# Optimization experiments

Hardware: AMD Instinct MI355X
Metric: run time of the kernel (lower is better)

Reference implementation:

```python
import jax, jax.numpy as jnp
import numpy as np

B, L, D = 2, 4096, 2048
H, K = 32, 16              # num_heads, mini_batch_size
HD = D // H                # head_dim = 64
NMB = L // K               # 256 mini-batches
TTT_BASE_LR = 1.0
LN_EPS = 1e-6


def setup_inputs() -> dict:
    key = jax.random.key(0)
    ks = jax.random.split(key, 16)
    r = lambda k, s: 0.02 * jax.random.normal(k, s, dtype=jnp.float32)
    return {
        "hidden_states": jax.random.normal(ks[0], (B, L, D), dtype=jnp.float32),
        "wq_w": r(ks[1], (D, D)), "wq_b": r(ks[2], (D,)),
        "wk_w": r(ks[3], (D, D)), "wk_b": r(ks[4], (D,)),
        "wv_w": r(ks[5], (D, D)), "wv_b": r(ks[6], (D,)),
        "wo_w": r(ks[7], (D, D)), "wo_b": r(ks[8], (D,)),
        "ttt_norm_weight": 1.0 + r(ks[9], (H, HD)),
        "ttt_norm_bias": r(ks[10], (H, HD)),
        "lr_w": r(ks[11], (H, 1, D)),       # learnable_ttt_lr_weight
        "lr_b": r(ks[12], (H, 1)),          # learnable_ttt_lr_bias
        "W1": r(ks[13], (H, HD, HD)),
        "b1": r(ks[14], (H, 1, HD)),
        "post_norm_w": jnp.ones((D,), jnp.float32),
        "post_norm_b": jnp.zeros((D,), jnp.float32),
    }


def ln_fwd(x, gamma, beta, eps=LN_EPS):
    mu = x.mean(-1, keepdims=True)
    var = ((x - mu) ** 2).mean(-1, keepdims=True)
    return gamma * ((x - mu) / jnp.sqrt(var + eps)) + beta


def ln_fused_l2_bwd(x, l2_target, gamma, beta, eps=LN_EPS):
    # grad of 0.5*||LN(x)*gamma+beta - target||^2 w.r.t. x (standard TTT helper)
    Dd = x.shape[-1]
    mu = x.mean(-1, keepdims=True)
    var = ((x - mu) ** 2).mean(-1, keepdims=True)
    std = jnp.sqrt(var + eps)
    x_hat = (x - mu) / std
    grad_x_hat = (gamma * x_hat + beta - l2_target) * gamma
    return (Dd * grad_x_hat
            - grad_x_hat.sum(-1, keepdims=True)
            - x_hat * (x_hat * grad_x_hat).sum(-1, keepdims=True)) / (Dd * std)


def reference(hidden_states, wq_w, wq_b, wk_w, wk_b, wv_w, wv_b, wo_w, wo_b,
              ttt_norm_weight, ttt_norm_bias, lr_w, lr_b, W1, b1,
              post_norm_w, post_norm_b):
    # QKV projections
    XQ = (hidden_states @ wq_w + wq_b).reshape(B, L, H, HD)
    XK = (hidden_states @ wk_w + wk_b).reshape(B, L, H, HD)
    XV = (hidden_states @ wv_w + wv_b).reshape(B, L, H, HD)
    # L2 normalize q/k per head (F.normalize, eps=1e-12)
    XQ = XQ / jnp.maximum(jnp.linalg.norm(XQ, axis=-1, keepdims=True), 1e-12)
    XK = XK / jnp.maximum(jnp.linalg.norm(XK, axis=-1, keepdims=True), 1e-12)
    # ln_reconstruction_target: torch.std is unbiased (ddof=1), eps added to std
    diff = XV - XK
    mu = diff.mean(-1, keepdims=True)
    std = jnp.std(diff, axis=-1, ddof=1, keepdims=True)
    XV = (ttt_norm_weight[None, None] * ((diff - mu) / (std + 1e-8))
          + ttt_norm_bias[None, None]) + XK
    # reshape to mini-batches: [B,H,NMB,K,HD]
    Xmb = hidden_states.reshape(B, NMB, K, D)
    tohd = lambda t: t.transpose(0, 2, 1, 3).reshape(B, H, NMB, K, HD)
    XQ, XK, XV = tohd(XQ), tohd(XK), tohd(XV)
    # eta gate: einsum('bnkc,hdc->bhnkd') with d==1, sigmoid, scale
    ttt_lr = jnp.einsum('bnkc,hdc->bhnkd', Xmb, lr_w) + lr_b.reshape(1, H, 1, 1, 1)
    ttt_lr = jax.nn.sigmoid(ttt_lr).transpose(0, 1, 2, 4, 3) * (TTT_BASE_LR / HD)  # [B,H,NMB,1,K]
    eta = jnp.broadcast_to(ttt_lr / K, (B, H, NMB, K, K))
    ln_w = ttt_norm_weight[:, None, :]  # [H,1,HD]
    ln_b = ttt_norm_bias[:, None, :]
    tril = jnp.tril(jnp.ones((K, K), jnp.float32))
    W1s = jnp.broadcast_to(W1[None], (B, H, HD, HD))
    b1s = jnp.broadcast_to(b1[None], (B, H, 1, HD))

    def step(carry, xs):
        W1c, b1c = carry
        xq, xk, xv, eta_mb = xs  # [B,H,K,HD], eta [B,H,K,K]
        Z1 = xk @ W1c + b1c
        grad = ln_fused_l2_bwd(Z1, xv - xk, ln_w, ln_b)        # [B,H,K,HD]
        Attn1 = tril * (xq @ xk.transpose(0, 1, 3, 2))         # causal within mini-batch
        b1_bar = b1c - (tril * eta_mb) @ grad
        Z1_bar = xq @ W1c - (eta_mb * Attn1) @ grad + b1_bar
        last_eta = eta_mb[:, :, -1, :, None]                   # [B,H,K,1]
        W1n = W1c - (last_eta * xk).transpose(0, 1, 3, 2) @ grad
        b1n = b1c - jnp.sum(last_eta * grad, axis=-2, keepdims=True)
        out = xq + ln_fwd(Z1_bar, ln_w, ln_b)
        return (W1n, b1n), out

    xs = tuple(t.transpose(2, 0, 1, 3, 4) for t in (XQ, XK, XV, eta))
    _, outs = jax.lax.scan(step, (W1s, b1s), xs)               # [NMB,B,H,K,HD]
    y = outs.transpose(1, 0, 3, 2, 4).reshape(B, L, D)
    # post_norm LayerNorm(eps=1e-6) then output projection
    mu = y.mean(-1, keepdims=True)
    var = ((y - mu) ** 2).mean(-1, keepdims=True)
    y = (y - mu) / jnp.sqrt(var + 1e-6) * post_norm_w + post_norm_b
    return y @ wo_w + wo_b
```

## Files before the change

### kernel.cpp

```cpp
#include <hip/hip_runtime.h>
#include <hip/hip_bf16.h>
#include <cstdint>
#include <cstddef>

#define DEV __device__ __forceinline__

constexpr int Bb = 2, Ls = 4096, Dd = 2048, Hh = 32, HD = 64, MBK = 16, NMBc = 256;
constexpr int MTOK = Bb * Ls;

typedef __bf16 bf16x8 __attribute__((ext_vector_type(8)));
typedef float  f32x4  __attribute__((ext_vector_type(4)));

DEV unsigned short f2bf(float f) {
    union { __bf16 h; unsigned short u; } x;
    x.h = (__bf16)f;
    return x.u;
}
DEV float b2f(unsigned short u) {
    union { unsigned int i; float f; } x; x.i = ((unsigned int)u) << 16;
    return x.f;
}

DEV float wsum64(float v) {
    int t;
    t = __builtin_amdgcn_update_dpp(0, __float_as_int(v), 0x111, 0xf, 0xf, true); v += __int_as_float(t);
    t = __builtin_amdgcn_update_dpp(0, __float_as_int(v), 0x112, 0xf, 0xf, true); v += __int_as_float(t);
    t = __builtin_amdgcn_update_dpp(0, __float_as_int(v), 0x114, 0xf, 0xf, true); v += __int_as_float(t);
    t = __builtin_amdgcn_update_dpp(0, __float_as_int(v), 0x118, 0xf, 0xf, true); v += __int_as_float(t);
    t = __builtin_amdgcn_update_dpp(0, __float_as_int(v), 0x142, 0xa, 0xf, true); v += __int_as_float(t);
    t = __builtin_amdgcn_update_dpp(0, __float_as_int(v), 0x143, 0xc, 0xf, true); v += __int_as_float(t);
    return __int_as_float(__builtin_amdgcn_readlane(__float_as_int(v), 63));
}

DEV float rsum16(float v) {
    int t;
    t = __builtin_amdgcn_update_dpp(0, __float_as_int(v), 0x121, 0xf, 0xf, true); v += __int_as_float(t);
    t = __builtin_amdgcn_update_dpp(0, __float_as_int(v), 0x122, 0xf, 0xf, true); v += __int_as_float(t);
    t = __builtin_amdgcn_update_dpp(0, __float_as_int(v), 0x124, 0xf, 0xf, true); v += __int_as_float(t);
    t = __builtin_amdgcn_update_dpp(0, __float_as_int(v), 0x128, 0xf, 0xf, true); v += __int_as_float(t);
    return v;
}

DEV float qsum4(float v) {
    int t;
    t = __builtin_amdgcn_update_dpp(0, __float_as_int(v), 0xB1, 0xf, 0xf, true); v += __int_as_float(t);
    t = __builtin_amdgcn_update_dpp(0, __float_as_int(v), 0x4E, 0xf, 0xf, true); v += __int_as_float(t);
    return v;
}

DEV float sel4(int n, float a, float b, float c, float d) {
    float v = (n == 1) ? b : a;
    v = (n == 2) ? c : v;
    v = (n == 3) ? d : v;
    return v;
}

DEV void g2l16(const void* g, void* l) {
    __builtin_amdgcn_global_load_lds(
        (__attribute__((address_space(1))) void*)(g),
        (__attribute__((address_space(3))) void*)(l), 16, 0, 0);
}

__global__ __launch_bounds__(256) void cast_hs_kernel(const float* __restrict__ src,
                                                      unsigned short* __restrict__ dst) {
    int i = (blockIdx.x * 256 + threadIdx.x) * 4;
    float4 v = *(const float4*)(src + i);
    ushort4 o; o.x = f2bf(v.x); o.y = f2bf(v.y); o.z = f2bf(v.z); o.w = f2bf(v.w);
    *(ushort4*)(dst + i) = o;
}

__global__ __launch_bounds__(256) void transpose_cast_kernel(const float* __restrict__ W,
                                                             unsigned short* __restrict__ Wt) {
    __shared__ float tile[64][65];
    int bx = blockIdx.x & 31;
    int by = blockIdx.x >> 5;
    int t = threadIdx.x;
    int r = t >> 4, c4 = (t & 15) * 4;
    #pragma unroll
    for (int i = 0; i < 4; ++i) {
        int row = r + i * 16;
        float4 v = *(const float4*)(W + (size_t)(bx * 64 + row) * Dd + by * 64 + c4);
        tile[row][c4 + 0] = v.x; tile[row][c4 + 1] = v.y;
        tile[row][c4 + 2] = v.z; tile[row][c4 + 3] = v.w;
    }
    __syncthreads();
    #pragma unroll
    for (int i = 0; i < 4; ++i) {
        int row = r + i * 16;
        ushort4 o;
        o.x = f2bf(tile[c4 + 0][row]); o.y = f2bf(tile[c4 + 1][row]);
        o.z = f2bf(tile[c4 + 2][row]); o.w = f2bf(tile[c4 + 3][row]);
        *(ushort4*)(Wt + (size_t)(by * 64 + row) * Dd + bx * 64 + c4) = o;
    }
}

__global__ __launch_bounds__(256) void gemm_bt_kernel(const unsigned short* __restrict__ A,
                                                      const unsigned short* __restrict__ Bt,
                                                      const float* __restrict__ bias,
                                                      float* __restrict__ C,
                                                      int M, int N, int Kd) {
    __shared__ unsigned short sA[128 * 64];
    __shared__ unsigned short sB[128 * 64];
    int t = threadIdx.x;
    int lane = t & 63;
    int wid = t >> 6, wm = wid >> 1, wn = wid & 1;
    int quad = lane >> 4, c = lane & 15;
    int bm = blockIdx.x, bn = blockIdx.y;

    const unsigned short* pa[4]; const unsigned short* pb[4];
    unsigned short* la[4]; unsigned short* lb[4];
    #pragma unroll
    for (int i = 0; i < 4; ++i) {
        int lin = i * 256 + t;
        int row = lin >> 3, blk = lin & 7;
        int oct = blk ^ (row & 7);
        pa[i] = A  + (size_t)(bm * 128 + row) * Kd + oct * 8;
        pb[i] = Bt + (size_t)(bn * 128 + row) * Kd + oct * 8;
        la[i] = sA + lin * 8;
        lb[i] = sB + lin * 8;
    }

    f32x4 acc[4][4];
    #pragma unroll
    for (int i = 0; i < 4; ++i)
        #pragma unroll
        for (int j = 0; j < 4; ++j)
            #pragma unroll
            for (int r = 0; r < 4; ++r) acc[i][j][r] = 0.f;

    const char* sAc = (const char*)sA;
    const char* sBc = (const char*)sB;
    int rowA0 = wm * 64 + c, rowB0 = wn * 64 + c;
    int sw = (c & 7);

    int nkt = Kd >> 6;
    for (int kt = 0; kt < nkt; ++kt) {
        #pragma unroll
        for (int i = 0; i < 4; ++i) {
            g2l16(pa[i], la[i]);
            g2l16(pb[i], lb[i]);
            pa[i] += 64; pb[i] += 64;
        }
        __syncthreads();
        #pragma unroll
        for (int s = 0; s < 2; ++s) {
            bf16x8 af[4], bfv[4];
            int so = (s << 2) | quad;
            #pragma unroll
            for (int mt = 0; mt < 4; ++mt)
                af[mt] = *(const bf16x8*)(sAc + (rowA0 + mt * 16) * 128 + ((so ^ sw) * 16));
            #pragma unroll
            for (int nt = 0; nt < 4; ++nt)
                bfv[nt] = *(const bf16x8*)(sBc + (rowB0 + nt * 16) * 128 + ((so ^ sw) * 16));
            #pragma unroll
            for (int mt = 0; mt < 4; ++mt)
                #pragma unroll
                for (int nt = 0; nt < 4; ++nt)
                    acc[mt][nt] = __builtin_amdgcn_mfma_f32_16x16x32_bf16(af[mt], bfv[nt], acc[mt][nt], 0, 0, 0);
        }
        __syncthreads();
    }

    float bv[4];
    #pragma unroll
    for (int nt = 0; nt < 4; ++nt) bv[nt] = bias[bn * 128 + wn * 64 + nt * 16 + c];
    #pragma unroll
    for (int mt = 0; mt < 4; ++mt)
        #pragma unroll
        for (int r = 0; r < 4; ++r) {
            int row = bm * 128 + wm * 64 + mt * 16 + quad * 4 + r;
            float* cp = C + (size_t)row * N + bn * 128 + wn * 64 + c;
            #pragma unroll
            for (int nt = 0; nt < 4; ++nt) cp[nt * 16] = acc[mt][nt][r] + bv[nt];
        }
}

__global__ __launch_bounds__(256) void lr_kernel(const float* __restrict__ hs,
                                                 const float* __restrict__ lrw,
                                                 const float* __restrict__ lrb,
                                                 float* __restrict__ lr_out) {
    int tok = blockIdx.x;
    int t = threadIdx.x;
    int h = t >> 3, j0 = t & 7;
    const float* row = hs + (size_t)tok * Dd;
    const float* wr = lrw + (size_t)h * Dd;
    float p = 0.f;
    for (int j = j0 * 4; j < Dd; j += 32) {
        float4 a = *(const float4*)(row + j);
        float4 w = *(const float4*)(wr + j);
        p += a.x * w.x + a.y * w.y + a.z * w.z + a.w * w.w;
    }
    __shared__ float red[32][8];
    red[h][j0] = p;
    __syncthreads();
    if (t < 32) {
        float s = 0.f;
        #pragma unroll
        for (int i = 0; i < 8; ++i) s += red[t][i];
        s += lrb[t];
        s = 1.f / (1.f + expf(-s));
        s *= 1.0f / (HD * MBK);
        int b = tok >> 12, l = tok & (Ls - 1);
        lr_out[(size_t)(b * Hh + t) * Ls + l] = s;
    }
}

__global__ __launch_bounds__(256) void attn_kernel(const float* __restrict__ XQ,
                                                   const float* __restrict__ XK,
                                                   const float* __restrict__ lrbuf,
                                                   unsigned short* __restrict__ attG) {
    __shared__ unsigned short qb[4][16 * 72];
    __shared__ unsigned short kb[4][16 * 72];
    int t = threadIdx.x, w = t >> 6, lane = t & 63;
    int gid = blockIdx.x * 4 + w;
    int bh = gid >> 8, nmb = gid & 255;
    int b = bh >> 5, h = bh & 31;
    int l0 = nmb * 16;
    int tok = lane >> 2, fq = lane & 3;
    size_t base = ((size_t)(b * Ls) + l0 + tok) * Dd + h * 64 + fq * 16;
    float4 qv[4], kv[4];
    #pragma unroll
    for (int i = 0; i < 4; ++i) {
        qv[i] = *(const float4*)(XQ + base + 4 * i);
        kv[i] = *(const float4*)(XK + base + 4 * i);
    }
    float sq = 0.f, sk = 0.f;
    #pragma unroll
    for (int i = 0; i < 4; ++i) {
        sq += qv[i].x * qv[i].x + qv[i].y * qv[i].y + qv[i].z * qv[i].z + qv[i].w * qv[i].w;
        sk += kv[i].x * kv[i].x + kv[i].y * kv[i].y + kv[i].z * kv[i].z + kv[i].w * kv[i].w;
    }
    float rq = 1.f / fmaxf(sqrtf(qsum4(sq)), 1e-12f);
    float rk = 1.f / fmaxf(sqrtf(qsum4(sk)), 1e-12f);
    #pragma unroll
    for (int i = 0; i < 4; ++i) {
        ushort4 oq, ok;
        oq.x = f2bf(qv[i].x * rq); oq.y = f2bf(qv[i].y * rq);
        oq.z = f2bf(qv[i].z * rq); oq.w = f2bf(qv[i].w * rq);
        ok.x = f2bf(kv[i].x * rk); ok.y = f2bf(kv[i].y * rk);
        ok.z = f2bf(kv[i].z * rk); ok.w = f2bf(kv[i].w * rk);
        *(ushort4*)&qb[w][tok * 72 + fq * 16 + 4 * i] = oq;
        *(ushort4*)&kb[w][tok * 72 + fq * 16 + 4 * i] = ok;
    }
    __syncthreads();
    int q2 = lane >> 4, n = lane & 15;
    bf16x8 qf0 = *(const bf16x8*)&qb[w][n * 72 + 8 * q2];
    bf16x8 qf1 = *(const bf16x8*)&qb[w][n * 72 + 32 + 8 * q2];
    bf16x8 kf0 = *(const bf16x8*)&kb[w][n * 72 + 8 * q2];
    bf16x8 kf1 = *(const bf16x8*)&kb[w][n * 72 + 32 + 8 * q2];
    const f32x4 zero4 = {0.f, 0.f, 0.f, 0.f};
    f32x4 a = __builtin_amdgcn_mfma_f32_16x16x32_bf16(qf1, kf1, zero4, 0, 0, 0);
    a = __builtin_amdgcn_mfma_f32_16x16x32_bf16(qf0, kf0, a, 0, 0, 0);
    float svn = lrbuf[(size_t)bh * Ls + l0 + n];
    unsigned short* op = attG + ((size_t)bh * NMBc + nmb) * 256;
    #pragma unroll
    for (int r = 0; r < 4; ++r) {
        int i = 4 * q2 + r;
        float v = (i >= n) ? (-svn * (a[r] + 1.f)) : 0.f;
        op[i * 16 + n] = f2bf(v);
    }
}

DEV void stage_qkv(float4 q, float4 k, float4 v,
                   float* tq, float* tk, float* tv,
                   unsigned short* bq, unsigned short* bk,
                   int rowp, int c4p, float4 lnw4, float4 lnb4) {
    float rq = 1.f / fmaxf(sqrtf(rsum16(q.x*q.x + q.y*q.y + q.z*q.z + q.w*q.w)), 1e-12f);
    q.x *= rq; q.y *= rq; q.z *= rq; q.w *= rq;
    float rk = 1.f / fmaxf(sqrtf(rsum16(k.x*k.x + k.y*k.y + k.z*k.z + k.w*k.w)), 1e-12f);
    k.x *= rk; k.y *= rk; k.z *= rk; k.w *= rk;
    float4 df; df.x = v.x - k.x; df.y = v.y - k.y; df.z = v.z - k.z; df.w = v.w - k.w;
    float mu = rsum16(df.x + df.y + df.z + df.w) * (1.f / 64.f);
    float4 cc; cc.x = df.x - mu; cc.y = df.y - mu; cc.z = df.z - mu; cc.w = df.w - mu;
    float var = rsum16(cc.x*cc.x + cc.y*cc.y + cc.z*cc.z + cc.w*cc.w) * (1.f / 63.f);
    float rs = 1.f / (sqrtf(var) + 1e-8f);
    float4 vn;
    vn.x = lnw4.x * cc.x * rs + lnb4.x + k.x;
    vn.y = lnw4.y * cc.y * rs + lnb4.y + k.y;
    vn.z = lnw4.z * cc.z * rs + lnb4.z + k.z;
    vn.w = lnw4.w * cc.w * rs + lnb4.w + k.w;
    *(float4*)&tq[rowp * 68 + c4p] = q;
    *(float4*)&tk[rowp * 68 + c4p] = k;
    *(float4*)&tv[rowp * 68 + c4p] = vn;
    ushort4 qb, kb;
    qb.x = f2bf(q.x); qb.y = f2bf(q.y); qb.z = f2bf(q.z); qb.w = f2bf(q.w);
    kb.x = f2bf(k.x); kb.y = f2bf(k.y); kb.z = f2bf(k.z); kb.w = f2bf(k.w);
    *(ushort4*)&bq[rowp * 72 + c4p] = qb;
    *(ushort4*)&bk[rowp * 72 + c4p] = kb;
}

__global__ __launch_bounds__(256, 1) void scan_kernel(const float* __restrict__ XQ,
                                                      const float* __restrict__ XK,
                                                      const float* __restrict__ XV,
                                                      const float* __restrict__ lrbuf,
                                                      const unsigned short* __restrict__ attG,
                                                      const float* __restrict__ W1in,
                                                      const float* __restrict__ b1in,
                                                      const float* __restrict__ lnw_g,
                                                      const float* __restrict__ lnb_g,
                                                      float* __restrict__ Y) {
    int bh = blockIdx.x;
    int b = bh >> 5, h = bh & 31;
    int t = threadIdx.x;
    int w = t >> 6;
    int lane = t & 63;
    int q = lane >> 4, n = lane & 15;
    int gc = 16 * w + n;

    __shared__ float tiles[2][3][16 * 68];
    __shared__ unsigned short tbq[2][16 * 72];
    __shared__ unsigned short tbk[2][16 * 72];
    __shared__ float svb[2][16];
    __shared__ unsigned short wt_hi[64 * 72];
    __shared__ unsigned short wt_lo[64 * 72];
    __shared__ float zTr[16 * 68];
    __shared__ unsigned short gbufT[64 * 32];
    __shared__ unsigned short sxkT[64 * 32];
    __shared__ unsigned short attb[16 * 32];
    __shared__ float pb[4 * 64];
    __shared__ float s1p[16 * 4], s2p[16 * 4];
    __shared__ float s1z[16 * 4], s2z[16 * 4];

    #pragma unroll
    for (int i = 0; i < 16; ++i) {
        int k = i * 4 + w;
        float val = W1in[(size_t)h * 4096 + (size_t)k * 64 + lane];
        unsigned short hi = f2bf(val);
        unsigned short lo = f2bf(val - b2f(hi));
        wt_hi[lane * 72 + k] = hi;
        wt_lo[lane * 72 + k] = lo;
    }
    #pragma unroll
    for (int i = 0; i < 8; ++i) { gbufT[i * 256 + t] = 0; sxkT[i * 256 + t] = 0; }
    #pragma unroll
    for (int i = 0; i < 2; ++i) attb[i * 256 + t] = 0;

    float b1r = b1in[h * 64 + lane];
    float b1c = b1in[h * 64 + gc];
    float lnwr = lnw_g[h * 64 + lane];
    float lnbr = lnb_g[h * 64 + lane];
    float lnwc = lnw_g[h * 64 + gc];
    float lnbc = lnb_g[h * 64 + gc];

    const size_t gbase = ((size_t)b * Ls) * Dd + h * 64;
    const float* lrp = lrbuf + (size_t)bh * Ls;
    const unsigned short* attp_base = attG + (size_t)bh * NMBc * 256;
    int arow = 4 * w + (lane >> 2), ac4 = (lane & 3) * 4;

    int rowp = t >> 4, c4p = (t & 15) * 4;
    float4 lnw4 = *(const float4*)(lnw_g + h * 64 + c4p);
    float4 lnb4 = *(const float4*)(lnb_g + h * 64 + c4p);

    {
        float4 q0 = *(const float4*)(XQ + gbase + (size_t)rowp * Dd + c4p);
        float4 k0 = *(const float4*)(XK + gbase + (size_t)rowp * Dd + c4p);
        float4 v0 = *(const float4*)(XV + gbase + (size_t)rowp * Dd + c4p);
        stage_qkv(q0, k0, v0, &tiles[0][0][0], &tiles[0][1][0], &tiles[0][2][0],
                  tbq[0], tbk[0], rowp, c4p, lnw4, lnb4);
    }
    if (t < 16) svb[0][t] = lrp[t];
    float4 preq = *(const float4*)(XQ + gbase + (size_t)(16 + rowp) * Dd + c4p);
    float4 prek = *(const float4*)(XK + gbase + (size_t)(16 + rowp) * Dd + c4p);
    float4 prev = *(const float4*)(XV + gbase + (size_t)(16 + rowp) * Dd + c4p);
    float presv = (t < 16) ? lrp[16 + t] : 0.f;
    ushort4 attp = {0, 0, 0, 0};
    if (lane < 16) attp = *(const ushort4*)(attp_base + arow * 16 + ac4);
    __syncthreads();

    const f32x4 zero4 = {0.f, 0.f, 0.f, 0.f};

    for (int nmb = 0; nmb < NMBc; ++nmb) {
        int cb = nmb & 1, nb2 = cb ^ 1;
        int l0 = nmb * 16;
        stage_qkv(preq, prek, prev, &tiles[nb2][0][0], &tiles[nb2][1][0], &tiles[nb2][2][0],
                  tbq[nb2], tbk[nb2], rowp, c4p, lnw4, lnb4);
        if (t < 16) svb[nb2][t] = presv;
        if (lane < 16) {
            *(ushort4*)&attb[arow * 32 + ac4] = attp;
            int ap = (nmb + 1 < NMBc) ? (nmb + 1) : (NMBc - 1);
            attp = *(const ushort4*)(attp_base + (size_t)ap * 256 + arow * 16 + ac4);
        }
        int lp = (l0 + 32 <= Ls - 16) ? (l0 + 32) : (Ls - 16);
        preq = *(const float4*)(XQ + gbase + (size_t)(lp + rowp) * Dd + c4p);
        prek = *(const float4*)(XK + gbase + (size_t)(lp + rowp) * Dd + c4p);
        prev = *(const float4*)(XV + gbase + (size_t)(lp + rowp) * Dd + c4p);
        presv = (t < 16) ? lrp[lp + t] : 0.f;

        const float* xqs = &tiles[cb][0][0];
        const float* xks = &tiles[cb][1][0];
        const float* xvs = &tiles[cb][2][0];
        const unsigned short* bqs = tbq[cb];
        const unsigned short* bks = tbk[cb];

        bf16x8 qf0 = *(const bf16x8*)&bqs[n * 72 + 8 * q];
        bf16x8 qf1 = *(const bf16x8*)&bqs[n * 72 + 32 + 8 * q];
        bf16x8 kf0 = *(const bf16x8*)&bks[n * 72 + 8 * q];
        bf16x8 kf1 = *(const bf16x8*)&bks[n * 72 + 32 + 8 * q];

        bf16x8 wh0 = *(const bf16x8*)&wt_hi[gc * 72 + 8 * q];
        bf16x8 wh1 = *(const bf16x8*)&wt_hi[gc * 72 + 32 + 8 * q];
        bf16x8 wl0 = *(const bf16x8*)&wt_lo[gc * 72 + 8 * q];
        bf16x8 wl1 = *(const bf16x8*)&wt_lo[gc * 72 + 32 + 8 * q];

        f32x4 z1 = __builtin_amdgcn_mfma_f32_16x16x32_bf16(kf0, wh0, zero4, 0, 0, 0);
        z1 = __builtin_amdgcn_mfma_f32_16x16x32_bf16(kf1, wh1, z1, 0, 0, 0);
        f32x4 z1l = __builtin_amdgcn_mfma_f32_16x16x32_bf16(kf0, wl0, zero4, 0, 0, 0);
        z1l = __builtin_amdgcn_mfma_f32_16x16x32_bf16(kf1, wl1, z1l, 0, 0, 0);
        z1 = z1 + z1l;
        f32x4 zb = __builtin_amdgcn_mfma_f32_16x16x32_bf16(qf0, wh0, zero4, 0, 0, 0);
        zb = __builtin_amdgcn_mfma_f32_16x16x32_bf16(qf1, wh1, zb, 0, 0, 0);
        f32x4 zbl = __builtin_amdgcn_mfma_f32_16x16x32_bf16(qf0, wl0, zero4, 0, 0, 0);
        zbl = __builtin_amdgcn_mfma_f32_16x16x32_bf16(qf1, wl1, zbl, 0, 0, 0);
        zb = zb + zbl;

        #pragma unroll
        for (int r = 0; r < 4; ++r) zTr[(4 * q + r) * 68 + gc] = z1[r];
        {
            float p1[4], p2[4];
            #pragma unroll
            for (int r = 0; r < 4; ++r) {
                float za = z1[r] + b1c;
                p1[r] = rsum16(za);
                p2[r] = rsum16(za * za);
            }
            if (n < 4) {
                s1p[(4 * q + n) * 4 + w] = sel4(n, p1[0], p1[1], p1[2], p1[3]);
                s2p[(4 * q + n) * 4 + w] = sel4(n, p2[0], p2[1], p2[2], p2[3]);
            }
        }
        __syncthreads();

        float xk_rm[4], xv_rm[4], zar[4];
        #pragma unroll
        for (int r = 0; r < 4; ++r) {
            int rw = 4 * w + r;
            zar[r] = zTr[rw * 68 + lane] + b1r;
            xk_rm[r] = xks[rw * 68 + lane];
            xv_rm[r] = xvs[rw * 68 + lane];
        }
        float4 svr4 = *(const float4*)&svb[cb][4 * w];
        float svr[4] = {svr4.x, svr4.y, svr4.z, svr4.w};
        float gr[4]; float pbv = 0.f;
        #pragma unroll
        for (int r = 0; r < 4; ++r) {
            int rw = 4 * w + r;
            float4 a1 = *(const float4*)&s1p[rw * 4];
            float4 a2 = *(const float4*)&s2p[rw * 4];
            float s1 = a1.x + a1.y + a1.z + a1.w;
            float s2 = a2.x + a2.y + a2.z + a2.w;
            float mu = s1 * (1.f / 64.f);
            float var = s2 * (1.f / 64.f) - mu * mu;
            float rstd = rsqrtf(var + 1e-6f);
            float xh = (zar[r] - mu) * rstd;
            float g = (lnwr * xh + lnbr - (xv_rm[r] - xk_rm[r])) * lnwr;
            float sg = wsum64(g);
            float sxg = wsum64(xh * g);
            gr[r] = (64.f * g - sg - xh * sxg) * rstd * (1.f / 64.f);
            pbv += svr[r] * gr[r];
        }
        {
            ushort4 gp, sp;
            gp.x = f2bf(gr[0]); gp.y = f2bf(gr[1]); gp.z = f2bf(gr[2]); gp.w = f2bf(gr[3]);
            sp.x = f2bf(svr[0] * xk_rm[0]); sp.y = f2bf(svr[1] * xk_rm[1]);
            sp.z = f2bf(svr[2] * xk_rm[2]); sp.w = f2bf(svr[3] * xk_rm[3]);
            *(ushort4*)&gbufT[lane * 32 + 4 * w] = gp;
            *(ushort4*)&sxkT[lane * 32 + 4 * w] = sp;
            pb[w * 64 + lane] = pbv;
        }
        __syncthreads();

        bf16x8 gF = *(const bf16x8*)&gbufT[gc * 32 + 8 * q];
        bf16x8 amF = *(const bf16x8*)&attb[n * 32 + 8 * q];
        zb = __builtin_amdgcn_mfma_f32_16x16x32_bf16(amF, gF, zb, 0, 0, 0);
        float zbar[4], xqc[4];
        {
            float pz1[4], pz2[4];
            #pragma unroll
            for (int r = 0; r < 4; ++r) {
                zbar[r] = zb[r] + b1c;
                pz1[r] = rsum16(zbar[r]);
                pz2[r] = rsum16(zbar[r] * zbar[r]);
                xqc[r] = xqs[(4 * q + r) * 68 + gc];
            }
            if (n < 4) {
                s1z[(4 * q + n) * 4 + w] = sel4(n, pz1[0], pz1[1], pz1[2], pz1[3]);
                s2z[(4 * q + n) * 4 + w] = sel4(n, pz2[0], pz2[1], pz2[2], pz2[3]);
            }
        }
        #pragma unroll
        for (int tm = 0; tm < 4; ++tm) {
            bf16x8 ax = *(const bf16x8*)&sxkT[(16 * tm + n) * 32 + 8 * q];
            f32x4 dl = __builtin_amdgcn_mfma_f32_16x16x32_bf16(ax, gF, zero4, 0, 0, 0);
            int ko = 16 * tm + 4 * q;
            ushort4 h4 = *(ushort4*)&wt_hi[gc * 72 + ko];
            ushort4 l4 = *(ushort4*)&wt_lo[gc * 72 + ko];
            float w0 = b2f(h4.x) + b2f(l4.x) - dl[0];
            float w1 = b2f(h4.y) + b2f(l4.y) - dl[1];
            float w2 = b2f(h4.z) + b2f(l4.z) - dl[2];
            float w3 = b2f(h4.w) + b2f(l4.w) - dl[3];
            h4.x = f2bf(w0); l4.x = f2bf(w0 - b2f(h4.x));
            h4.y = f2bf(w1); l4.y = f2bf(w1 - b2f(h4.y));
            h4.z = f2bf(w2); l4.z = f2bf(w2 - b2f(h4.z));
            h4.w = f2bf(w3); l4.w = f2bf(w3 - b2f(h4.w));
            *(ushort4*)&wt_hi[gc * 72 + ko] = h4;
            *(ushort4*)&wt_lo[gc * 72 + ko] = l4;
        }
        float b1r_n = b1r - (pb[0 * 64 + lane] + pb[64 + lane] +
                             pb[128 + lane] + pb[192 + lane]);
        float b1c_n = b1c - (pb[0 * 64 + gc] + pb[64 + gc] +
                             pb[128 + gc] + pb[192 + gc]);
        __syncthreads();

        #pragma unroll
        for (int r = 0; r < 4; ++r) {
            int row = 4 * q + r;
            float4 a1 = *(const float4*)&s1z[row * 4];
            float4 a2 = *(const float4*)&s2z[row * 4];
            float s1 = a1.x + a1.y + a1.z + a1.w;
            float s2 = a2.x + a2.y + a2.z + a2.w;
            float mu = s1 * (1.f / 64.f);
            float var = s2 * (1.f / 64.f) - mu * mu;
            float rstd = rsqrtf(var + 1e-6f);
            float o = lnwc * ((zbar[r] - mu) * rstd) + lnbc + xqc[r];
            Y[gbase + (size_t)(l0 + row) * Dd + gc] = o;
        }
        b1r = b1r_n; b1c = b1c_n;
    }
}

__global__ __launch_bounds__(256) void postnorm_kernel(const float* __restrict__ Y,
                                                       const float* __restrict__ pw,
                                                       const float* __restrict__ pb,
                                                       unsigned short* __restrict__ Yb) {
    int tok = blockIdx.x, t = threadIdx.x;
    const float* row = Y + (size_t)tok * Dd;
    int c0 = t * 4, c1 = 1024 + t * 4;
    float4 v0 = *(const float4*)(row + c0);
    float4 v1 = *(const float4*)(row + c1);
    float s1 = v0.x + v0.y + v0.z + v0.w + v1.x + v1.y + v1.z + v1.w;
    float s2 = v0.x * v0.x + v0.y * v0.y + v0.z * v0.z + v0.w * v0.w +
               v1.x * v1.x + v1.y * v1.y + v1.z * v1.z + v1.w * v1.w;
    s1 = wsum64(s1); s2 = wsum64(s2);
    __shared__ float r1[4], r2[4];
    if ((t & 63) == 0) { r1[t >> 6] = s1; r2[t >> 6] = s2; }
    __syncthreads();
    float S1 = r1[0] + r1[1] + r1[2] + r1[3];
    float S2 = r2[0] + r2[1] + r2[2] + r2[3];
    float mu = S1 * (1.f / 2048.f);
    float var = S2 * (1.f / 2048.f) - mu * mu;
    float rstd = rsqrtf(var + 1e-6f);
    float4 w0 = *(const float4*)(pw + c0), b0 = *(const float4*)(pb + c0);
    float4 w1 = *(const float4*)(pw + c1), b1 = *(const float4*)(pb + c1);
    ushort4 o0, o1;
    o0.x = f2bf((v0.x - mu) * rstd * w0.x + b0.x);
    o0.y = f2bf((v0.y - mu) * rstd * w0.y + b0.y);
    o0.z = f2bf((v0.z - mu) * rstd * w0.z + b0.z);
    o0.w = f2bf((v0.w - mu) * rstd * w0.w + b0.w);
    o1.x = f2bf((v1.x - mu) * rstd * w1.x + b1.x);
    o1.y = f2bf((v1.y - mu) * rstd * w1.y + b1.y);
    o1.z = f2bf((v1.z - mu) * rstd * w1.z + b1.z);
    o1.w = f2bf((v1.w - mu) * rstd * w1.w + b1.w);
    *(ushort4*)(Yb + (size_t)tok * Dd + c0) = o0;
    *(ushort4*)(Yb + (size_t)tok * Dd + c1) = o1;
}

extern "C" void kernel_launch(void* const* d_in, const int* in_sizes, int n_in,
                              void* d_out, int out_size, void* d_ws, size_t ws_size,
                              hipStream_t stream) {
    const float* hs   = (const float*)d_in[0];
    const float* wq_w = (const float*)d_in[1];
    const float* wq_b = (const float*)d_in[2];
    const float* wk_w = (const float*)d_in[3];
    const float* wk_b = (const float*)d_in[4];
    const float* wv_w = (const float*)d_in[5];
    const float* wv_b = (const float*)d_in[6];
    const float* wo_w = (const float*)d_in[7];
    const float* wo_b = (const float*)d_in[8];
    const float* lnw  = (const float*)d_in[9];
    const float* lnb  = (const float*)d_in[10];
    const float* lr_w = (const float*)d_in[11];
    const float* lr_b = (const float*)d_in[12];
    const float* W1   = (const float*)d_in[13];
    const float* b1   = (const float*)d_in[14];
    const float* pnw  = (const float*)d_in[15];
    const float* pnb  = (const float*)d_in[16];
    float* out = (float*)d_out;

    char* ws = (char*)d_ws;
    size_t off = 0;
    auto alloc = [&](size_t bytes) -> void* {
        void* p = ws + off; off += (bytes + 255) & ~(size_t)255; return p;
    };
    unsigned short* hsb = (unsigned short*)alloc((size_t)MTOK * Dd * 2);
    unsigned short* wtb = (unsigned short*)alloc((size_t)Dd * Dd * 2);
    float* XQ = (float*)alloc((size_t)MTOK * Dd * 4);
    float* XK = (float*)alloc((size_t)MTOK * Dd * 4);
    float* XV = (float*)alloc((size_t)MTOK * Dd * 4);
    float* lrbuf = (float*)alloc((size_t)Bb * Hh * Ls * 4);
    float* Y = XQ;
    unsigned short* Yb = hsb;
    unsigned short* attG = hsb;

    dim3 blk(256);
    cast_hs_kernel<<<dim3(MTOK * Dd / 1024), blk, 0, stream>>>(hs, hsb);

    transpose_cast_kernel<<<dim3(1024), blk, 0, stream>>>(wq_w, wtb);
    gemm_bt_kernel<<<dim3(64, 16), blk, 0, stream>>>(hsb, wtb, wq_b, XQ, MTOK, Dd, Dd);
    transpose_cast_kernel<<<dim3(1024), blk, 0, stream>>>(wk_w, wtb);
    gemm_bt_kernel<<<dim3(64, 16), blk, 0, stream>>>(hsb, wtb, wk_b, XK, MTOK, Dd, Dd);
    transpose_cast_kernel<<<dim3(1024), blk, 0, stream>>>(wv_w, wtb);
    gemm_bt_kernel<<<dim3(64, 16), blk, 0, stream>>>(hsb, wtb, wv_b, XV, MTOK, Dd, Dd);

    lr_kernel<<<dim3(MTOK), blk, 0, stream>>>(hs, lr_w, lr_b, lrbuf);
    attn_kernel<<<dim3(Bb * Hh * NMBc / 4), blk, 0, stream>>>(XQ, XK, lrbuf, attG);

    scan_kernel<<<dim3(Bb * Hh), blk, 0, stream>>>(XQ, XK, XV, lrbuf, attG, W1, b1, lnw, lnb, Y);

    postnorm_kernel<<<dim3(MTOK), blk, 0, stream>>>(Y, pnw, pnb, Yb);

    transpose_cast_kernel<<<dim3(1024), blk, 0, stream>>>(wo_w, wtb);
    gemm_bt_kernel<<<dim3(64, 16), blk, 0, stream>>>(Yb, wtb, wo_b, out, MTOK, Dd, Dd);
}
```

Measured before the change: 1.448 ms.

## Fuse attention-matrix computation into scan kernel and defer output LN store

Removes the separate attn_kernel and its global attG buffer; warp 0 of the scan kernel now computes the masked eta-scaled q·k^T tile with MFMA inside each mini-batch step, into double-buffered shared memory. The final LayerNorm and store of each mini-batch's output is deferred to the next iteration so one __syncthreads per step can be dropped. Prefetch loads for the next tiles are moved later in the loop. This removes one launch and a global round trip, but adds serial MFMA work to the latency-bound scan loop, which runs on only 64 blocks.

```diff
diff --git a/kernel.cpp b/kernel.cpp
--- a/kernel.cpp
+++ b/kernel.cpp
@@ -38,13 +38,6 @@
     t = __builtin_amdgcn_update_dpp(0, __float_as_int(v), 0x122, 0xf, 0xf, true); v += __int_as_float(t);
     t = __builtin_amdgcn_update_dpp(0, __float_as_int(v), 0x124, 0xf, 0xf, true); v += __int_as_float(t);
     t = __builtin_amdgcn_update_dpp(0, __float_as_int(v), 0x128, 0xf, 0xf, true); v += __int_as_float(t);
-    return v;
-}
-
-DEV float qsum4(float v) {
-    int t;
-    t = __builtin_amdgcn_update_dpp(0, __float_as_int(v), 0xB1, 0xf, 0xf, true); v += __int_as_float(t);
-    t = __builtin_amdgcn_update_dpp(0, __float_as_int(v), 0x4E, 0xf, 0xf, true); v += __int_as_float(t);
     return v;
 }
 
@@ -202,62 +195,6 @@
         s *= 1.0f / (HD * MBK);
         int b = tok >> 12, l = tok & (Ls - 1);
         lr_out[(size_t)(b * Hh + t) * Ls + l] = s;
-    }
-}
-
-__global__ __launch_bounds__(256) void attn_kernel(const float* __restrict__ XQ,
-                                                   const float* __restrict__ XK,
-                                                   const float* __restrict__ lrbuf,
-                                                   unsigned short* __restrict__ attG) {
-    __shared__ unsigned short qb[4][16 * 72];
-    __shared__ unsigned short kb[4][16 * 72];
-    int t = threadIdx.x, w = t >> 6, lane = t & 63;
-    int gid = blockIdx.x * 4 + w;
-    int bh = gid >> 8, nmb = gid & 255;
-    int b = bh >> 5, h = bh & 31;
-    int l0 = nmb * 16;
-    int tok = lane >> 2, fq = lane & 3;
-    size_t base = ((size_t)(b * Ls) + l0 + tok) * Dd + h * 64 + fq * 16;
-    float4 qv[4], kv[4];
-    #pragma unroll
-    for (int i = 0; i < 4; ++i) {
-        qv[i] = *(const float4*)(XQ + base + 4 * i);
-        kv[i] = *(const float4*)(XK + base + 4 * i);
-    }
-    float sq = 0.f, sk = 0.f;
-    #pragma unroll
-    for (int i = 0; i < 4; ++i) {
-        sq += qv[i].x * qv[i].x + qv[i].y * qv[i].y + qv[i].z * qv[i].z + qv[i].w * qv[i].w;
-        sk += kv[i].x * kv[i].x + kv[i].y * kv[i].y + kv[i].z * kv[i].z + kv[i].w * kv[i].w;
-    }
-    float rq = 1.f / fmaxf(sqrtf(qsum4(sq)), 1e-12f);
-    float rk = 1.f / fmaxf(sqrtf(qsum4(sk)), 1e-12f);
-    #pragma unroll
-    for (int i = 0; i < 4; ++i) {
-        ushort4 oq, ok;
-        oq.x = f2bf(qv[i].x * rq); oq.y = f2bf(qv[i].y * rq);
-        oq.z = f2bf(qv[i].z * rq); oq.w = f2bf(qv[i].w * rq);
-        ok.x = f2bf(kv[i].x * rk); ok.y = f2bf(kv[i].y * rk);
-        ok.z = f2bf(kv[i].z * rk); ok.w = f2bf(kv[i].w * rk);
-        *(ushort4*)&qb[w][tok * 72 + fq * 16 + 4 * i] = oq;
-        *(ushort4*)&kb[w][tok * 72 + fq * 16 + 4 * i] = ok;
-    }
-    __syncthreads();
-    int q2 = lane >> 4, n = lane & 15;
-    bf16x8 qf0 = *(const bf16x8*)&qb[w][n * 72 + 8 * q2];
-    bf16x8 qf1 = *(const bf16x8*)&qb[w][n * 72 + 32 + 8 * q2];
-    bf16x8 kf0 = *(const bf16x8*)&kb[w][n * 72 + 8 * q2];
-    bf16x8 kf1 = *(const bf16x8*)&kb[w][n * 72 + 32 + 8 * q2];
-    const f32x4 zero4 = {0.f, 0.f, 0.f, 0.f};
-    f32x4 a = __builtin_amdgcn_mfma_f32_16x16x32_bf16(qf1, kf1, zero4, 0, 0, 0);
-    a = __builtin_amdgcn_mfma_f32_16x16x32_bf16(qf0, kf0, a, 0, 0, 0);
-    float svn = lrbuf[(size_t)bh * Ls + l0 + n];
-    unsigned short* op = attG + ((size_t)bh * NMBc + nmb) * 256;
-    #pragma unroll
-    for (int r = 0; r < 4; ++r) {
-        int i = 4 * q2 + r;
-        float v = (i >= n) ? (-svn * (a[r] + 1.f)) : 0.f;
-        op[i * 16 + n] = f2bf(v);
     }
 }
 
@@ -293,7 +230,6 @@
                                                       const float* __restrict__ XK,
                                                       const float* __restrict__ XV,
                                                       const float* __restrict__ lrbuf,
-                                                      const unsigned short* __restrict__ attG,
                                                       const float* __restrict__ W1in,
                                                       const float* __restrict__ b1in,
                                                       const float* __restrict__ lnw_g,
@@ -316,7 +252,7 @@
     __shared__ float zTr[16 * 68];
     __shared__ unsigned short gbufT[64 * 32];
     __shared__ unsigned short sxkT[64 * 32];
-    __shared__ unsigned short attb[16 * 32];
+    __shared__ unsigned short attb[2][16 * 32];
     __shared__ float pb[4 * 64];
     __shared__ float s1p[16 * 4], s2p[16 * 4];
     __shared__ float s1z[16 * 4], s2z[16 * 4];
@@ -333,7 +269,7 @@
     #pragma unroll
     for (int i = 0; i < 8; ++i) { gbufT[i * 256 + t] = 0; sxkT[i * 256 + t] = 0; }
     #pragma unroll
-    for (int i = 0; i < 2; ++i) attb[i * 256 + t] = 0;
+    for (int i = 0; i < 4; ++i) attb[0][0] , ((unsigned short*)attb)[i * 256 + t] = 0;
 
     float b1r = b1in[h * 64 + lane];
     float b1c = b1in[h * 64 + gc];
@@ -344,8 +280,6 @@
 
     const size_t gbase = ((size_t)b * Ls) * Dd + h * 64;
     const float* lrp = lrbuf + (size_t)bh * Ls;
-    const unsigned short* attp_base = attG + (size_t)bh * NMBc * 256;
-    int arow = 4 * w + (lane >> 2), ac4 = (lane & 3) * 4;
 
     int rowp = t >> 4, c4p = (t & 15) * 4;
     float4 lnw4 = *(const float4*)(lnw_g + h * 64 + c4p);
@@ -363,11 +297,11 @@
     float4 prek = *(const float4*)(XK + gbase + (size_t)(16 + rowp) * Dd + c4p);
     float4 prev = *(const float4*)(XV + gbase + (size_t)(16 + rowp) * Dd + c4p);
     float presv = (t < 16) ? lrp[16 + t] : 0.f;
-    ushort4 attp = {0, 0, 0, 0};
-    if (lane < 16) attp = *(const ushort4*)(attp_base + arow * 16 + ac4);
     __syncthreads();
 
     const f32x4 zero4 = {0.f, 0.f, 0.f, 0.f};
+    float zbar_p[4] = {0.f, 0.f, 0.f, 0.f};
+    float xqc_p[4]  = {0.f, 0.f, 0.f, 0.f};
 
     for (int nmb = 0; nmb < NMBc; ++nmb) {
         int cb = nmb & 1, nb2 = cb ^ 1;
@@ -375,16 +309,6 @@
         stage_qkv(preq, prek, prev, &tiles[nb2][0][0], &tiles[nb2][1][0], &tiles[nb2][2][0],
                   tbq[nb2], tbk[nb2], rowp, c4p, lnw4, lnb4);
         if (t < 16) svb[nb2][t] = presv;
-        if (lane < 16) {
-            *(ushort4*)&attb[arow * 32 + ac4] = attp;
-            int ap = (nmb + 1 < NMBc) ? (nmb + 1) : (NMBc - 1);
-            attp = *(const ushort4*)(attp_base + (size_t)ap * 256 + arow * 16 + ac4);
-        }
-        int lp = (l0 + 32 <= Ls - 16) ? (l0 + 32) : (Ls - 16);
-        preq = *(const float4*)(XQ + gbase + (size_t)(lp + rowp) * Dd + c4p);
-        prek = *(const float4*)(XK + gbase + (size_t)(lp + rowp) * Dd + c4p);
-        prev = *(const float4*)(XV + gbase + (size_t)(lp + rowp) * Dd + c4p);
-        presv = (t < 16) ? lrp[lp + t] : 0.f;
 
         const float* xqs = &tiles[cb][0][0];
         const float* xks = &tiles[cb][1][0];
@@ -428,15 +352,43 @@
                 s2p[(4 * q + n) * 4 + w] = sel4(n, p2[0], p2[1], p2[2], p2[3]);
             }
         }
+        if (w == 0) {
+            f32x4 aacc = __builtin_amdgcn_mfma_f32_16x16x32_bf16(qf1, kf1, zero4, 0, 0, 0);
+            aacc = __builtin_amdgcn_mfma_f32_16x16x32_bf16(qf0, kf0, aacc, 0, 0, 0);
+            float svn = svb[cb][n];
+            #pragma unroll
+            for (int r = 0; r < 4; ++r) {
+                int i = 4 * q + r;
+                attb[cb][i * 32 + n] = f2bf((i >= n) ? (-svn * (aacc[r] + 1.f)) : 0.f);
+            }
+        }
         __syncthreads();
 
-        float xk_rm[4], xv_rm[4], zar[4];
+        if (nmb > 0) {
+            int l0p = l0 - 16;
+            #pragma unroll
+            for (int r = 0; r < 4; ++r) {
+                int row = 4 * q + r;
+                float4 a1 = *(const float4*)&s1z[row * 4];
+                float4 a2 = *(const float4*)&s2z[row * 4];
+                float s1 = a1.x + a1.y + a1.z + a1.w;
+                float s2 = a2.x + a2.y + a2.z + a2.w;
+                float mu = s1 * (1.f / 64.f);
+                float var = s2 * (1.f / 64.f) - mu * mu;
+                float rstd = rsqrtf(var + 1e-6f);
+                float o = lnwc * ((zbar_p[r] - mu) * rstd) + lnbc + xqc_p[r];
+                Y[gbase + (size_t)(l0p + row) * Dd + gc] = o;
+            }
+        }
+
+        float xk_rm[4], xv_rm[4], zar[4], xqc[4];
         #pragma unroll
         for (int r = 0; r < 4; ++r) {
             int rw = 4 * w + r;
             zar[r] = zTr[rw * 68 + lane] + b1r;
             xk_rm[r] = xks[rw * 68 + lane];
             xv_rm[r] = xvs[rw * 68 + lane];
+            xqc[r] = xqs[(4 * q + r) * 68 + gc];
         }
         float4 svr4 = *(const float4*)&svb[cb][4 * w];
         float svr[4] = {svr4.x, svr4.y, svr4.z, svr4.w};
@@ -469,10 +421,16 @@
         }
         __syncthreads();
 
+        int lp = (l0 + 32 <= Ls - 16) ? (l0 + 32) : (Ls - 16);
+        preq = *(const float4*)(XQ + gbase + (size_t)(lp + rowp) * Dd + c4p);
+        prek = *(const float4*)(XK + gbase + (size_t)(lp + rowp) * Dd + c4p);
+        prev = *(const float4*)(XV + gbase + (size_t)(lp + rowp) * Dd + c4p);
+        presv = (t < 16) ? lrp[lp + t] : 0.f;
+
         bf16x8 gF = *(const bf16x8*)&gbufT[gc * 32 + 8 * q];
-        bf16x8 amF = *(const bf16x8*)&attb[n * 32 + 8 * q];
+        bf16x8 amF = *(const bf16x8*)&attb[cb][n * 32 + 8 * q];
         zb = __builtin_amdgcn_mfma_f32_16x16x32_bf16(amF, gF, zb, 0, 0, 0);
-        float zbar[4], xqc[4];
+        float zbar[4];
         {
             float pz1[4], pz2[4];
             #pragma unroll
@@ -480,7 +438,6 @@
                 zbar[r] = zb[r] + b1c;
                 pz1[r] = rsum16(zbar[r]);
                 pz2[r] = rsum16(zbar[r] * zbar[r]);
-                xqc[r] = xqs[(4 * q + r) * 68 + gc];
             }
             if (n < 4) {
                 s1z[(4 * q + n) * 4 + w] = sel4(n, pz1[0], pz1[1], pz1[2], pz1[3]);
@@ -509,8 +466,14 @@
                              pb[128 + lane] + pb[192 + lane]);
         float b1c_n = b1c - (pb[0 * 64 + gc] + pb[64 + gc] +
                              pb[128 + gc] + pb[192 + gc]);
-        __syncthreads();
-
+        #pragma unroll
+        for (int r = 0; r < 4; ++r) { zbar_p[r] = zbar[r]; xqc_p[r] = xqc[r]; }
+        b1r = b1r_n; b1c = b1c_n;
+    }
+
+    __syncthreads();
+    {
+        int l0p = (NMBc - 1) * 16;
         #pragma unroll
         for (int r = 0; r < 4; ++r) {
             int row = 4 * q + r;
@@ -521,10 +484,9 @@
             float mu = s1 * (1.f / 64.f);
             float var = s2 * (1.f / 64.f) - mu * mu;
             float rstd = rsqrtf(var + 1e-6f);
-            float o = lnwc * ((zbar[r] - mu) * rstd) + lnbc + xqc[r];
-            Y[gbase + (size_t)(l0 + row) * Dd + gc] = o;
-        }
-        b1r = b1r_n; b1c = b1c_n;
+            float o = lnwc * ((zbar_p[r] - mu) * rstd) + lnbc + xqc_p[r];
+            Y[gbase + (size_t)(l0p + row) * Dd + gc] = o;
+        }
     }
 }
 
@@ -599,7 +561,6 @@
     float* lrbuf = (float*)alloc((size_t)Bb * Hh * Ls * 4);
     float* Y = XQ;
     unsigned short* Yb = hsb;
-    unsigned short* attG = hsb;
 
     dim3 blk(256);
     cast_hs_kernel<<<dim3(MTOK * Dd / 1024), blk, 0, stream>>>(hs, hsb);
@@ -612,9 +573,8 @@
     gemm_bt_kernel<<<dim3(64, 16), blk, 0, stream>>>(hsb, wtb, wv_b, XV, MTOK, Dd, Dd);
 
     lr_kernel<<<dim3(MTOK), blk, 0, stream>>>(hs, lr_w, lr_b, lrbuf);
-    attn_kernel<<<dim3(Bb * Hh * NMBc / 4), blk, 0, stream>>>(XQ, XK, lrbuf, attG);
-
-    scan_kernel<<<dim3(Bb * Hh), blk, 0, stream>>>(XQ, XK, XV, lrbuf, attG, W1, b1, lnw, lnb, Y);
+
+    scan_kernel<<<dim3(Bb * Hh), blk, 0, stream>>>(XQ, XK, XV, lrbuf, W1, b1, lnw, lnb, Y);
 
     postnorm_kernel<<<dim3(MTOK), blk, 0, stream>>>(Y, pnw, pnb, Yb);
 
```

New measurement: 1.434 ms. Within noise of the previous version (-0.9%).
